# Performance work log

Measured on AMD Instinct MI355X. Metric: run time of the kernel, lower is better.

The kernel has to match this reference:

```python
import jax, jax.numpy as jnp
import numpy as np

D_K = 64
SCALE = jnp.sqrt(jnp.float32(D_K))

def setup_inputs() -> dict:
    key = jax.random.key(0)
    kq, kk, kv = jax.random.split(key, 3)
    shape = (2, 16, 2048, D_K)  # [batch, heads, seq, d_k]
    return {
        "Q": jax.random.normal(kq, shape, dtype=jnp.float32),
        "K": jax.random.normal(kk, shape, dtype=jnp.float32),
        "V": jax.random.normal(kv, shape, dtype=jnp.float32),
    }

def reference(Q, K, V):
    # scores: [B, H, S, S]
    scores = jnp.einsum("bhqd,bhkd->bhqk", Q, K) / SCALE
    weights = jax.nn.softmax(scores, axis=-1)
    return jnp.einsum("bhqk,bhkd->bhqd", weights, V)
```

## Files before the change

kernel.cpp:

```cpp
#include <hip/hip_runtime.h>
#include <math.h>

#define S_LEN 2048
#define DK 64
#define BH 32
#define BK 64
#define NT 32
#define TILE_US 8192
#define TILE_B  16384

#if defined(__has_builtin)
#if __has_builtin(__builtin_amdgcn_exp2f)
#define EXP2F(x) __builtin_amdgcn_exp2f(x)
#else
#define EXP2F(x) exp2f(x)
#endif
#else
#define EXP2F(x) exp2f(x)
#endif

typedef _Float16 f16x8 __attribute__((ext_vector_type(8)));
typedef __fp16   fp16x2 __attribute__((ext_vector_type(2)));
typedef float    f32x16 __attribute__((ext_vector_type(16)));

#define MFMAH(a,b,c) __builtin_amdgcn_mfma_f32_32x32x16_f16((a),(b),(c),0,0,0)

union U16H { uint4 u; f16x8 h; unsigned short s[8]; };

__device__ __forceinline__ f16x8 asf16(uint4 u){ U16H t; t.u = u; return t.h; }
__device__ __forceinline__ f16x8 u4h(unsigned a, unsigned b, unsigned c, unsigned d){
    U16H t; t.u = make_uint4(a,b,c,d); return t.h;
}
__device__ __forceinline__ unsigned pk16(float a, float b){
    union { fp16x2 h; unsigned u; } c;
    c.h = __builtin_amdgcn_cvt_pkrtz(a, b);
    return c.u;
}
__device__ __forceinline__ unsigned short f16b(float x){
    union { _Float16 f; unsigned short s; } c; c.f = (_Float16)x; return c.s;
}

__global__ __launch_bounds__(256) void prep2(const float* __restrict__ K,
                                             const float* __restrict__ V,
                                             unsigned short* __restrict__ W) {
    const int t = threadIdx.x;
    const int head = blockIdx.x >> 5;
    const int kb = blockIdx.x & 31;
    const size_t tbase = (size_t)head * S_LEN * DK + (size_t)kb * BK * DK;
    unsigned short* Wt = W + (size_t)(head * NT + kb) * TILE_US;

    #pragma unroll
    for (int i = 0; i < 2; ++i) {
        const int P = i * 256 + t;
        const int ks = P >> 7, rhi = (P >> 6) & 1, q5 = (P >> 5) & 1, r31 = P & 31;
        const float* kp = K + tbase + (size_t)(rhi * 32 + r31) * DK + ks * 16 + q5 * 8;
        const float4 a = *(const float4*)kp;
        const float4 b = *(const float4*)(kp + 4);
        *(uint4*)(Wt + P * 8) = make_uint4(pk16(a.x, a.y), pk16(a.z, a.w),
                                           pk16(b.x, b.y), pk16(b.z, b.w));
    }
    #pragma unroll
    for (int i = 0; i < 2; ++i) {
        const int P = i * 256 + t;
        const int ks = P >> 7, dhi = (P >> 6) & 1, q5 = (P >> 5) & 1, d31 = P & 31;
        const int d = dhi * 32 + d31;
        const float* vp = V + tbase + (size_t)(ks * 16 + q5 * 8) * DK + d;
        U16H o;
        #pragma unroll
        for (int j = 0; j < 8; ++j) o.s[j] = f16b(vp[(size_t)j * DK]);
        *(uint4*)(Wt + 4096 + P * 8) = o.u;
    }
}

__global__ __launch_bounds__(256) void fa6(const float* __restrict__ Q,
                                           const unsigned short* __restrict__ W,
                                           float* __restrict__ O) {
    __shared__ __align__(16) float Rg[2][32][68];
    __shared__ float Lp[3][32];

    const int tid = threadIdx.x;
    const int kh  = tid >> 6;
    const int lane = tid & 63;
    const int L31 = tid & 31;
    const int q5  = (tid >> 5) & 1;

    const int bid  = blockIdx.x;
    const int x    = bid & 7, g = bid >> 3;
    const int head = ((g >> 6) << 3) | x;
    const int strip = g & 63;
    const size_t hbase = (size_t)head * S_LEN * DK;
    const unsigned short* Wk = W + (size_t)head * NT * TILE_US;
    const unsigned short* Wv = Wk + 4096;

    const float c1 = 0.18033688011112042f;
    f16x8 qf[4];
    {
        const int qrow = strip * 32 + L31;
        const float* qp = Q + hbase + (size_t)qrow * DK;
        #pragma unroll
        for (int ks = 0; ks < 4; ++ks) {
            const float4 a = *(const float4*)(qp + ks * 16 + q5 * 8);
            const float4 b = *(const float4*)(qp + ks * 16 + q5 * 8 + 4);
            qf[ks] = u4h(pk16(a.x * c1, a.y * c1), pk16(a.z * c1, a.w * c1),
                         pk16(b.x * c1, b.y * c1), pk16(b.z * c1, b.w * c1));
        }
    }

    f32x16 accO0 = {}, accO1 = {};
    float lsum = 0.f;

    for (int it = 0; it < 8; ++it) {
        const int kb = kh * 8 + it;
        const unsigned short* Kt = Wk + (size_t)kb * TILE_US;
        const unsigned short* Vt = Wv + (size_t)kb * TILE_US;

        uint4 ka0[4], ka1[4];
        #pragma unroll
        for (int ks = 0; ks < 4; ++ks) {
            ka0[ks] = *(const uint4*)(Kt + ks * 1024 + lane * 8);
            ka1[ks] = *(const uint4*)(Kt + ks * 1024 + 512 + lane * 8);
        }

        f32x16 s0 = {}, s1 = {};
        #pragma unroll
        for (int ks = 0; ks < 4; ++ks) {
            s0 = MFMAH(asf16(ka0[ks]), qf[ks], s0);
            s1 = MFMAH(asf16(ka1[ks]), qf[ks], s1);
        }

        uint4 va0[4], va1[4];
        #pragma unroll
        for (int ks = 0; ks < 4; ++ks) {
            va0[ks] = *(const uint4*)(Vt + ks * 1024 + lane * 8);
            va1[ks] = *(const uint4*)(Vt + ks * 1024 + 512 + lane * 8);
        }

        #pragma unroll
        for (int r = 0; r < 16; ++r) {
            s0[r] = EXP2F(s0[r]); lsum += s0[r];
            s1[r] = EXP2F(s1[r]); lsum += s1[r];
        }

        unsigned P2[2][4][2];
        #pragma unroll
        for (int b = 0; b < 4; ++b) {
            P2[0][b][0] = pk16(s0[4*b+0], s0[4*b+1]);
            P2[0][b][1] = pk16(s0[4*b+2], s0[4*b+3]);
            P2[1][b][0] = pk16(s1[4*b+0], s1[4*b+1]);
            P2[1][b][1] = pk16(s1[4*b+2], s1[4*b+3]);
        }

        #pragma unroll
        for (int ks = 0; ks < 4; ++ks) {
            const int mt = ks >> 1, kk2 = (ks & 1) * 2;
            const unsigned own0 = q5 ? P2[mt][kk2+1][0] : P2[mt][kk2][0];
            const unsigned own1 = q5 ? P2[mt][kk2+1][1] : P2[mt][kk2][1];
            const unsigned snd0 = q5 ? P2[mt][kk2][0]   : P2[mt][kk2+1][0];
            const unsigned snd1 = q5 ? P2[mt][kk2][1]   : P2[mt][kk2+1][1];
            const unsigned r0 = (unsigned)__shfl_xor((int)snd0, 32);
            const unsigned r1 = (unsigned)__shfl_xor((int)snd1, 32);
            const f16x8 ph = q5 ? u4h(r0, r1, own0, own1) : u4h(own0, own1, r0, r1);

            accO0 = MFMAH(asf16(va0[ks]), ph, accO0);
            accO1 = MFMAH(asf16(va1[ks]), ph, accO1);
        }
    }

    const float lw = lsum + __shfl_xor(lsum, 32);

    if (kh == 1 || kh == 3) {
        float* rp = &Rg[kh >> 1][L31][0];
        #pragma unroll
        for (int b = 0; b < 4; ++b) {
            *(float4*)(rp + 8 * b + 4 * q5) =
                make_float4(accO0[4*b+0], accO0[4*b+1], accO0[4*b+2], accO0[4*b+3]);
            *(float4*)(rp + 32 + 8 * b + 4 * q5) =
                make_float4(accO1[4*b+0], accO1[4*b+1], accO1[4*b+2], accO1[4*b+3]);
        }
    }
    if (kh >= 1 && q5 == 0) Lp[kh - 1][L31] = lw;
    __syncthreads();
    if (kh == 0 || kh == 2) {
        const float* rp = &Rg[kh >> 1][L31][0];
        #pragma unroll
        for (int b = 0; b < 4; ++b) {
            const float4 m0 = *(const float4*)(rp + 8 * b + 4 * q5);
            accO0[4*b+0] += m0.x; accO0[4*b+1] += m0.y; accO0[4*b+2] += m0.z; accO0[4*b+3] += m0.w;
            const float4 m1 = *(const float4*)(rp + 32 + 8 * b + 4 * q5);
            accO1[4*b+0] += m1.x; accO1[4*b+1] += m1.y; accO1[4*b+2] += m1.z; accO1[4*b+3] += m1.w;
        }
    }
    __syncthreads();
    if (kh == 2) {
        float* rp = &Rg[0][L31][0];
        #pragma unroll
        for (int b = 0; b < 4; ++b) {
            *(float4*)(rp + 8 * b + 4 * q5) =
                make_float4(accO0[4*b+0], accO0[4*b+1], accO0[4*b+2], accO0[4*b+3]);
            *(float4*)(rp + 32 + 8 * b + 4 * q5) =
                make_float4(accO1[4*b+0], accO1[4*b+1], accO1[4*b+2], accO1[4*b+3]);
        }
    }
    __syncthreads();
    if (kh == 0) {
        const float* rp = &Rg[0][L31][0];
        const float l = lw + Lp[0][L31] + Lp[1][L31] + Lp[2][L31];
        const float inv = 1.f / l;
        const int qrow = strip * 32 + L31;
        float* op = O + hbase + (size_t)qrow * DK;
        #pragma unroll
        for (int b = 0; b < 4; ++b) {
            const float4 m0 = *(const float4*)(rp + 8 * b + 4 * q5);
            float4 o0;
            o0.x = (accO0[4*b+0] + m0.x) * inv; o0.y = (accO0[4*b+1] + m0.y) * inv;
            o0.z = (accO0[4*b+2] + m0.z) * inv; o0.w = (accO0[4*b+3] + m0.w) * inv;
            *(float4*)(op + 8 * b + 4 * q5) = o0;
            const float4 m1 = *(const float4*)(rp + 32 + 8 * b + 4 * q5);
            float4 o1;
            o1.x = (accO1[4*b+0] + m1.x) * inv; o1.y = (accO1[4*b+1] + m1.y) * inv;
            o1.z = (accO1[4*b+2] + m1.z) * inv; o1.w = (accO1[4*b+3] + m1.w) * inv;
            *(float4*)(op + 32 + 8 * b + 4 * q5) = o1;
        }
    }
}

extern "C" void kernel_launch(void* const* d_in, const int* in_sizes, int n_in,
                              void* d_out, int out_size, void* d_ws, size_t ws_size,
                              hipStream_t stream) {
    const float* Q = (const float*)d_in[0];
    const float* K = (const float*)d_in[1];
    const float* V = (const float*)d_in[2];
    float* O = (float*)d_out;
    unsigned short* W = (unsigned short*)d_ws;
    prep2<<<dim3(BH * NT), dim3(256), 0, stream>>>(K, V, W);
    fa6<<<dim3(2048), dim3(256), 0, stream>>>(Q, W, O);
}
```

Baseline: 146.5 us.

## Stage K/V tiles in LDS via async global-to-LDS loads shared across query strips

The attention kernel now handles 64 query rows per block: two waves cover two 32-row strips and share each K/V tile, while two key-halves split the sequence. K/V tiles of 32 keys are double-buffered in shared memory using global_load_lds and prefetched one step ahead. Before this, every wave read K/V straight from global memory into registers. The prep kernel is relaid for 32-key tiles and the final reduction drops to a single exchange between two key-halves. This halves global K/V traffic per query row and overlaps the loads with compute, at the cost of a block barrier on every iteration and half as many blocks.

After: 161.1 us. 9.9% more time.

```diff
diff --git a/kernel.cpp b/kernel.cpp
--- a/kernel.cpp
+++ b/kernel.cpp
@@ -4,10 +4,9 @@
 #define S_LEN 2048
 #define DK 64
 #define BH 32
-#define BK 64
-#define NT 32
-#define TILE_US 8192
-#define TILE_B  16384
+#define NT32 64
+#define T32_US 4096
+#define T32_B 8192
 
 #if defined(__has_builtin)
 #if __has_builtin(__builtin_amdgcn_exp2f)
@@ -27,7 +26,9 @@
 
 union U16H { uint4 u; f16x8 h; unsigned short s[8]; };
 
-__device__ __forceinline__ f16x8 asf16(uint4 u){ U16H t; t.u = u; return t.h; }
+__device__ __forceinline__ f16x8 ldsh8(const unsigned short* p){
+    U16H t; t.u = *(const uint4*)p; return t.h;
+}
 __device__ __forceinline__ f16x8 u4h(unsigned a, unsigned b, unsigned c, unsigned d){
     U16H t; t.u = make_uint4(a,b,c,d); return t.h;
 }
@@ -39,63 +40,63 @@
 __device__ __forceinline__ unsigned short f16b(float x){
     union { _Float16 f; unsigned short s; } c; c.f = (_Float16)x; return c.s;
 }
-
-__global__ __launch_bounds__(256) void prep2(const float* __restrict__ K,
+__device__ __forceinline__ void gl_lds16(const void* g, void* l){
+    __builtin_amdgcn_global_load_lds(
+        (const __attribute__((address_space(1))) void*)g,
+        (__attribute__((address_space(3))) void*)l, 16, 0, 0);
+}
+
+__global__ __launch_bounds__(256) void prep3(const float* __restrict__ K,
                                              const float* __restrict__ V,
                                              unsigned short* __restrict__ W) {
     const int t = threadIdx.x;
-    const int head = blockIdx.x >> 5;
-    const int kb = blockIdx.x & 31;
-    const size_t tbase = (size_t)head * S_LEN * DK + (size_t)kb * BK * DK;
-    unsigned short* Wt = W + (size_t)(head * NT + kb) * TILE_US;
-
-    #pragma unroll
-    for (int i = 0; i < 2; ++i) {
-        const int P = i * 256 + t;
-        const int ks = P >> 7, rhi = (P >> 6) & 1, q5 = (P >> 5) & 1, r31 = P & 31;
-        const float* kp = K + tbase + (size_t)(rhi * 32 + r31) * DK + ks * 16 + q5 * 8;
+    const int head = blockIdx.x >> 6;
+    const int kb = blockIdx.x & 63;
+    const size_t tbase = (size_t)head * S_LEN * DK + (size_t)kb * 32 * DK;
+    unsigned short* Wt = W + (size_t)(head * NT32 + kb) * T32_US;
+
+    {
+        const int ks = t >> 6, q5 = (t >> 5) & 1, r31 = t & 31;
+        const float* kp = K + tbase + (size_t)r31 * DK + ks * 16 + q5 * 8;
         const float4 a = *(const float4*)kp;
         const float4 b = *(const float4*)(kp + 4);
-        *(uint4*)(Wt + P * 8) = make_uint4(pk16(a.x, a.y), pk16(a.z, a.w),
+        *(uint4*)(Wt + t * 8) = make_uint4(pk16(a.x, a.y), pk16(a.z, a.w),
                                            pk16(b.x, b.y), pk16(b.z, b.w));
     }
-    #pragma unroll
-    for (int i = 0; i < 2; ++i) {
-        const int P = i * 256 + t;
-        const int ks = P >> 7, dhi = (P >> 6) & 1, q5 = (P >> 5) & 1, d31 = P & 31;
-        const int d = dhi * 32 + d31;
-        const float* vp = V + tbase + (size_t)(ks * 16 + q5 * 8) * DK + d;
+    {
+        const int kv = t >> 7, dhi = (t >> 6) & 1, q5 = (t >> 5) & 1, d31 = t & 31;
+        const float* vp = V + tbase + (size_t)(kv * 16 + q5 * 8) * DK + dhi * 32 + d31;
         U16H o;
         #pragma unroll
         for (int j = 0; j < 8; ++j) o.s[j] = f16b(vp[(size_t)j * DK]);
-        *(uint4*)(Wt + 4096 + P * 8) = o.u;
-    }
-}
-
-__global__ __launch_bounds__(256) void fa6(const float* __restrict__ Q,
+        *(uint4*)(Wt + 2048 + t * 8) = o.u;
+    }
+}
+
+__global__ __launch_bounds__(256) void fa8(const float* __restrict__ Q,
                                            const unsigned short* __restrict__ W,
                                            float* __restrict__ O) {
-    __shared__ __align__(16) float Rg[2][32][68];
-    __shared__ float Lp[3][32];
+    __shared__ __align__(16) unsigned short SB[2][2][T32_US];
 
     const int tid = threadIdx.x;
-    const int kh  = tid >> 6;
+    const int w   = tid >> 6;
+    const int kh  = w >> 1;
+    const int st  = w & 1;
     const int lane = tid & 63;
     const int L31 = tid & 31;
     const int q5  = (tid >> 5) & 1;
 
     const int bid  = blockIdx.x;
     const int x    = bid & 7, g = bid >> 3;
-    const int head = ((g >> 6) << 3) | x;
-    const int strip = g & 63;
+    const int head = ((g >> 5) << 3) | x;
+    const int qb   = g & 31;
     const size_t hbase = (size_t)head * S_LEN * DK;
-    const unsigned short* Wk = W + (size_t)head * NT * TILE_US;
-    const unsigned short* Wv = Wk + 4096;
+    const unsigned short* Wh = W + (size_t)head * NT32 * T32_US;
 
     const float c1 = 0.18033688011112042f;
     f16x8 qf[4];
     {
-        const int qrow = strip * 32 + L31;
+        const int qrow = qb * 64 + st * 32 + L31;
         const float* qp = Q + hbase + (size_t)qrow * DK;
         #pragma unroll
         for (int ks = 0; ks < 4; ++ks) {
@@ -106,70 +107,69 @@
         }
     }
 
+    const int th = st * 64 + lane;
+
+    {
+        const char* src = (const char*)Wh + (size_t)(kh * 32) * T32_B + th * 16;
+        char* dst = (char*)&SB[kh][0][0] + th * 16;
+        #pragma unroll
+        for (int j = 0; j < 4; ++j) gl_lds16(src + j * 2048, dst + j * 2048);
+    }
+    __syncthreads();
+
     f32x16 accO0 = {}, accO1 = {};
     float lsum = 0.f;
 
-    for (int it = 0; it < 8; ++it) {
-        const int kb = kh * 8 + it;
-        const unsigned short* Kt = Wk + (size_t)kb * TILE_US;
-        const unsigned short* Vt = Wv + (size_t)kb * TILE_US;
-
-        uint4 ka0[4], ka1[4];
+    for (int it = 0; it < 32; ++it) {
+        const int cur = it & 1;
+        if (it + 1 < 32) {
+            const char* src = (const char*)Wh + (size_t)(kh * 32 + it + 1) * T32_B + th * 16;
+            char* dst = (char*)&SB[kh][cur ^ 1][0] + th * 16;
+            #pragma unroll
+            for (int j = 0; j < 4; ++j) gl_lds16(src + j * 2048, dst + j * 2048);
+        }
+        const unsigned short* B0 = &SB[kh][cur][0];
+
+        f32x16 s0 = {};
         #pragma unroll
         for (int ks = 0; ks < 4; ++ks) {
-            ka0[ks] = *(const uint4*)(Kt + ks * 1024 + lane * 8);
-            ka1[ks] = *(const uint4*)(Kt + ks * 1024 + 512 + lane * 8);
-        }
-
-        f32x16 s0 = {}, s1 = {};
-        #pragma unroll
-        for (int ks = 0; ks < 4; ++ks) {
-            s0 = MFMAH(asf16(ka0[ks]), qf[ks], s0);
-            s1 = MFMAH(asf16(ka1[ks]), qf[ks], s1);
-        }
-
-        uint4 va0[4], va1[4];
-        #pragma unroll
-        for (int ks = 0; ks < 4; ++ks) {
-            va0[ks] = *(const uint4*)(Vt + ks * 1024 + lane * 8);
-            va1[ks] = *(const uint4*)(Vt + ks * 1024 + 512 + lane * 8);
-        }
-
-        #pragma unroll
-        for (int r = 0; r < 16; ++r) {
-            s0[r] = EXP2F(s0[r]); lsum += s0[r];
-            s1[r] = EXP2F(s1[r]); lsum += s1[r];
-        }
-
-        unsigned P2[2][4][2];
+            const f16x8 a0 = ldsh8(B0 + (ks * 64 + q5 * 32 + L31) * 8);
+            s0 = MFMAH(a0, qf[ks], s0);
+        }
+
+        #pragma unroll
+        for (int r = 0; r < 16; ++r) { s0[r] = EXP2F(s0[r]); lsum += s0[r]; }
+
+        unsigned P2[4][2];
         #pragma unroll
         for (int b = 0; b < 4; ++b) {
-            P2[0][b][0] = pk16(s0[4*b+0], s0[4*b+1]);
-            P2[0][b][1] = pk16(s0[4*b+2], s0[4*b+3]);
-            P2[1][b][0] = pk16(s1[4*b+0], s1[4*b+1]);
-            P2[1][b][1] = pk16(s1[4*b+2], s1[4*b+3]);
-        }
-
-        #pragma unroll
-        for (int ks = 0; ks < 4; ++ks) {
-            const int mt = ks >> 1, kk2 = (ks & 1) * 2;
-            const unsigned own0 = q5 ? P2[mt][kk2+1][0] : P2[mt][kk2][0];
-            const unsigned own1 = q5 ? P2[mt][kk2+1][1] : P2[mt][kk2][1];
-            const unsigned snd0 = q5 ? P2[mt][kk2][0]   : P2[mt][kk2+1][0];
-            const unsigned snd1 = q5 ? P2[mt][kk2][1]   : P2[mt][kk2+1][1];
+            P2[b][0] = pk16(s0[4*b+0], s0[4*b+1]);
+            P2[b][1] = pk16(s0[4*b+2], s0[4*b+3]);
+        }
+
+        #pragma unroll
+        for (int kv = 0; kv < 2; ++kv) {
+            const int g0 = kv * 2, g1 = kv * 2 + 1;
+            const unsigned own0 = q5 ? P2[g1][0] : P2[g0][0];
+            const unsigned own1 = q5 ? P2[g1][1] : P2[g0][1];
+            const unsigned snd0 = q5 ? P2[g0][0] : P2[g1][0];
+            const unsigned snd1 = q5 ? P2[g0][1] : P2[g1][1];
             const unsigned r0 = (unsigned)__shfl_xor((int)snd0, 32);
             const unsigned r1 = (unsigned)__shfl_xor((int)snd1, 32);
             const f16x8 ph = q5 ? u4h(r0, r1, own0, own1) : u4h(own0, own1, r0, r1);
 
-            accO0 = MFMAH(asf16(va0[ks]), ph, accO0);
-            accO1 = MFMAH(asf16(va1[ks]), ph, accO1);
-        }
+            const f16x8 v0 = ldsh8(B0 + 2048 + (kv * 128 +       q5 * 32 + L31) * 8);
+            const f16x8 v1 = ldsh8(B0 + 2048 + (kv * 128 + 64 +  q5 * 32 + L31) * 8);
+            accO0 = MFMAH(v0, ph, accO0);
+            accO1 = MFMAH(v1, ph, accO1);
+        }
+        __syncthreads();
     }
 
     const float lw = lsum + __shfl_xor(lsum, 32);
-
-    if (kh == 1 || kh == 3) {
-        float* rp = &Rg[kh >> 1][L31][0];
+    float* Rg = (float*)SB;
+    float* rp = Rg + (st * 32 + L31) * 68;
+    if (kh == 1) {
         #pragma unroll
         for (int b = 0; b < 4; ++b) {
             *(float4*)(rp + 8 * b + 4 * q5) =
@@ -177,36 +177,12 @@
             *(float4*)(rp + 32 + 8 * b + 4 * q5) =
                 make_float4(accO1[4*b+0], accO1[4*b+1], accO1[4*b+2], accO1[4*b+3]);
         }
-    }
-    if (kh >= 1 && q5 == 0) Lp[kh - 1][L31] = lw;
-    __syncthreads();
-    if (kh == 0 || kh == 2) {
-        const float* rp = &Rg[kh >> 1][L31][0];
-        #pragma unroll
-        for (int b = 0; b < 4; ++b) {
-            const float4 m0 = *(const float4*)(rp + 8 * b + 4 * q5);
-            accO0[4*b+0] += m0.x; accO0[4*b+1] += m0.y; accO0[4*b+2] += m0.z; accO0[4*b+3] += m0.w;
-            const float4 m1 = *(const float4*)(rp + 32 + 8 * b + 4 * q5);
-            accO1[4*b+0] += m1.x; accO1[4*b+1] += m1.y; accO1[4*b+2] += m1.z; accO1[4*b+3] += m1.w;
-        }
-    }
-    __syncthreads();
-    if (kh == 2) {
-        float* rp = &Rg[0][L31][0];
-        #pragma unroll
-        for (int b = 0; b < 4; ++b) {
-            *(float4*)(rp + 8 * b + 4 * q5) =
-                make_float4(accO0[4*b+0], accO0[4*b+1], accO0[4*b+2], accO0[4*b+3]);
-            *(float4*)(rp + 32 + 8 * b + 4 * q5) =
-                make_float4(accO1[4*b+0], accO1[4*b+1], accO1[4*b+2], accO1[4*b+3]);
-        }
+        if (q5 == 0) rp[64] = lw;
     }
     __syncthreads();
     if (kh == 0) {
-        const float* rp = &Rg[0][L31][0];
-        const float l = lw + Lp[0][L31] + Lp[1][L31] + Lp[2][L31];
-        const float inv = 1.f / l;
-        const int qrow = strip * 32 + L31;
+        const float inv = 1.f / (lw + rp[64]);
+        const int qrow = qb * 64 + st * 32 + L31;
         float* op = O + hbase + (size_t)qrow * DK;
         #pragma unroll
         for (int b = 0; b < 4; ++b) {
@@ -232,6 +208,6 @@
     const float* V = (const float*)d_in[2];
     float* O = (float*)d_out;
     unsigned short* W = (unsigned short*)d_ws;
-    prep2<<<dim3(BH * NT), dim3(256), 0, stream>>>(K, V, W);
-    fa6<<<dim3(2048), dim3(256), 0, stream>>>(Q, W, O);
-}
+    prep3<<<dim3(BH * NT32), dim3(256), 0, stream>>>(K, V, W);
+    fa8<<<dim3(1024), dim3(256), 0, stream>>>(Q, W, O);
+}
```
